# Optimization experiments

Measured on AMD Instinct MI355X. Metric: run time of the kernel, lower is better.

## Reference

```python
import jax, jax.numpy as jnp
import numpy as np

N, D, H = 50000, 256, 8
HD = D // H
E = 800000
NEG_SLOPE = 0.2


def setup_inputs() -> dict:
    key = jax.random.key(0)
    ks = jax.random.split(key, 12)
    s = 1.0 / np.sqrt(D)
    return {
        "x": jax.random.normal(ks[0], (N, D), jnp.float32),
        "edge_index": jax.random.randint(ks[1], (2, E), 0, N, jnp.int64),
        "edge_attr": jax.random.normal(ks[2], (E, 16), jnp.float32),
        # GATConv params: lin weight (no bias), attention vectors, output bias
        "W": jax.random.normal(ks[3], (D, D), jnp.float32) * s,
        "att_src": jax.random.normal(ks[4], (H, HD), jnp.float32) * s,
        "att_dst": jax.random.normal(ks[5], (H, HD), jnp.float32) * s,
        "bias": jnp.zeros((D,), jnp.float32),
        # LayerNorm
        "ln_g": jnp.ones((D,), jnp.float32),
        "ln_b": jnp.zeros((D,), jnp.float32),
        # FFN
        "W1": jax.random.normal(ks[6], (D, D), jnp.float32) * s,
        "b1": jnp.zeros((D,), jnp.float32),
        "W2": jax.random.normal(ks[7], (D, D), jnp.float32) * s,
        "b2": jnp.zeros((D,), jnp.float32),
    }


def _gat_layer(x, edge_index, W, att_src, att_dst, bias, ln_g, ln_b, W1, b1, W2, b2):
    n = x.shape[0]
    # GATConv default add_self_loops=True
    sl = jnp.arange(n, dtype=edge_index.dtype)
    src = jnp.concatenate([edge_index[0], sl])  # [E+N]
    dst = jnp.concatenate([edge_index[1], sl])  # [E+N]

    xp = (x @ W).reshape(n, H, HD)                      # [N,H,hd]
    a_src = jnp.einsum("nhd,hd->nh", xp, att_src)        # [N,H]
    a_dst = jnp.einsum("nhd,hd->nh", xp, att_dst)        # [N,H]

    e = a_src[src] + a_dst[dst]                          # [E+N,H]
    e = jax.nn.leaky_relu(e, NEG_SLOPE)
    # segment softmax over destination nodes (every node has a self loop)
    m = jax.ops.segment_max(e, dst, num_segments=n)      # [N,H]
    ex = jnp.exp(e - m[dst])
    denom = jax.ops.segment_sum(ex, dst, num_segments=n) # [N,H]
    alpha = ex / (denom[dst] + 1e-16)                    # [E+N,H]

    msg = alpha[:, :, None] * xp[src]                    # [E+N,H,hd]
    out = jax.ops.segment_sum(msg, dst, num_segments=n)  # [N,H,hd]
    h = out.reshape(n, D) + bias

    # residual + LayerNorm
    r = h + x
    mu = jnp.mean(r, axis=-1, keepdims=True)
    var = jnp.mean(jnp.square(r - mu), axis=-1, keepdims=True)
    hn = (r - mu) / jnp.sqrt(var + 1e-5) * ln_g + ln_b

    # FFN
    return jax.nn.relu(hn @ W1 + b1) @ W2 + b2


def reference(x, edge_index, edge_attr, W, att_src, att_dst, bias, ln_g, ln_b, W1, b1, W2, b2):
    # edge_attr is accepted but unused (GATConv built without edge_dim)
    return _gat_layer(x, edge_index, W, att_src, att_dst, bias, ln_g, ln_b, W1, b1, W2, b2)
```

## Files before the change

### kernel.cpp

```cpp
#include <hip/hip_runtime.h>
#include <hip/hip_bf16.h>

#define H 8
#define HD 32
#define DD 256
#define NEG_SLOPE 0.2f
#define SLOT 64

typedef short bf16x8 __attribute__((ext_vector_type(8)));
typedef float f32x4 __attribute__((ext_vector_type(4)));

__device__ __forceinline__ unsigned short f2bf(float f) {
    unsigned int u = __float_as_uint(f);
    unsigned int r = (u + 0x7fffu + ((u >> 16) & 1u)) >> 16;
    return (unsigned short)r;
}
__device__ __forceinline__ float bf2f(unsigned short b) {
    return __uint_as_float(((unsigned int)b) << 16);
}

#define GLOAD_LDS16(g, s)                                                        \
    __builtin_amdgcn_global_load_lds((const __attribute__((address_space(1))) void*)(g), \
                                     (__attribute__((address_space(3))) void*)(s), 16, 0, 0)

__global__ __launch_bounds__(256) void zero_cnt(int* __restrict__ cnt, int N) {
    int i = blockIdx.x * 256 + threadIdx.x;
    if (i < N) cnt[i] = 0;
}

__global__ __launch_bounds__(256) void prep(const float* __restrict__ x, unsigned short* __restrict__ xb,
                                            const float* __restrict__ W, unsigned short* __restrict__ Wt,
                                            const float* __restrict__ W1, unsigned short* __restrict__ W1t,
                                            const float* __restrict__ W2, unsigned short* __restrict__ W2t,
                                            const int* __restrict__ ei, int* __restrict__ src_sorted,
                                            int* __restrict__ cnt, int N, int n4, int E, int HB) {
    int b = blockIdx.x;
    int tid = threadIdx.x;
    if (b < HB) {
        int e = b * 256 + tid;
        if (e < E) {
            int s = ei[e];
            int d = ei[E + e];
            int r = atomicAdd(&cnt[d], 1);
            if (r < SLOT) src_sorted[(size_t)d * SLOT + r] = s;
        }
    } else if (b < HB + 768) {
        int wb = b - HB;
        const float* src = (wb < 256) ? W : (wb < 512) ? W1 : W2;
        unsigned short* dst = (wb < 256) ? Wt : (wb < 512) ? W1t : W2t;
        int i = (wb & 255) * 256 + tid;
        int n = i >> 8, k = i & 255;
        dst[i] = f2bf(src[k * 256 + n]);
    } else {
        int i = (b - HB - 768) * 256 + tid;
        if (i < n4) {
            float4 v = ((const float4*)x)[i];
            ushort4 o;
            o.x = f2bf(v.x); o.y = f2bf(v.y); o.z = f2bf(v.z); o.w = f2bf(v.w);
            ((ushort4*)xb)[i] = o;
        }
    }
}

template <bool ATTN, bool PHASE2>
__global__ __launch_bounds__(256) void gemm_fused(
    const unsigned short* __restrict__ A,
    const unsigned short* __restrict__ B1t, const float* __restrict__ b1,
    const unsigned short* __restrict__ B2t, const float* __restrict__ b2,
    void* __restrict__ Cout, int M,
    const float* __restrict__ att_s, const float* __restrict__ att_d,
    float* __restrict__ a_srcO, float* __restrict__ a_dstO) {
    __shared__ __align__(16) unsigned short Als[16384];
    __shared__ __align__(16) unsigned short t1ls[PHASE2 ? 64 * 280 : 8];

    const int tid = threadIdx.x;
    const int l = tid & 63;
    const int w = tid >> 6;
    const int r16 = l & 15, q0 = l >> 4;
    const int row0 = blockIdx.x * 64;

#pragma unroll
    for (int k = 0; k < 8; k++) {
        int c = k * 256 + tid;
        const unsigned short* g = A + (size_t)min(row0 + (c & 63), M - 1) * DD + (c >> 6) * 8;
        GLOAD_LDS16(g, &Als[c * 8]);
    }
    __syncthreads();

    f32x4 zero = {0.f, 0.f, 0.f, 0.f};
    f32x4 acc[4][4];
#pragma unroll
    for (int i = 0; i < 4; i++)
#pragma unroll
        for (int j = 0; j < 4; j++) acc[i][j] = zero;

#pragma unroll
    for (int kk = 0; kk < 4; kk++) {
#pragma unroll
        for (int t = 0; t < 2; t++) {
            const int qq = kk * 8 + t * 4 + q0;
            bf16x8 af[4], bf[4];
#pragma unroll
            for (int j = 0; j < 4; j++)
                bf[j] = *(const bf16x8*)&B1t[(size_t)(w * 64 + j * 16 + r16) * DD + qq * 8];
#pragma unroll
            for (int i = 0; i < 4; i++)
                af[i] = *(const bf16x8*)&Als[(qq * 64 + i * 16 + r16) * 8];
#pragma unroll
            for (int i = 0; i < 4; i++)
#pragma unroll
                for (int j = 0; j < 4; j++)
                    acc[i][j] = __builtin_amdgcn_mfma_f32_16x16x32_bf16(af[i], bf[j], acc[i][j], 0, 0, 0);
        }
    }

    if (!PHASE2) {
        float aws0, aws1, aws2, aws3, awd0, awd1, awd2, awd3;
        int hA = 0, hB = 0;
        if (ATTN) {
            hA = w * 2; hB = hA + 1;
            aws0 = att_s[hA * HD + r16];
            aws1 = att_s[hA * HD + 16 + r16];
            aws2 = att_s[hB * HD + r16];
            aws3 = att_s[hB * HD + 16 + r16];
            awd0 = att_d[hA * HD + r16];
            awd1 = att_d[hA * HD + 16 + r16];
            awd2 = att_d[hB * HD + r16];
            awd3 = att_d[hB * HD + 16 + r16];
        }
#pragma unroll
        for (int i = 0; i < 4; i++) {
#pragma unroll
            for (int r = 0; r < 4; r++) {
                int row = row0 + i * 16 + q0 * 4 + r;
                if (row < M) {
#pragma unroll
                    for (int j = 0; j < 4; j++) {
                        int col = w * 64 + j * 16 + r16;
                        ((unsigned short*)Cout)[(size_t)row * DD + col] = f2bf(acc[i][j][r]);
                    }
                }
                if (ATTN) {
                    float v0 = acc[i][0][r], v1 = acc[i][1][r];
                    float v2 = acc[i][2][r], v3 = acc[i][3][r];
                    float ps0 = v0 * aws0 + v1 * aws1;
                    float ps1 = v2 * aws2 + v3 * aws3;
                    float pd0 = v0 * awd0 + v1 * awd1;
                    float pd1 = v2 * awd2 + v3 * awd3;
#pragma unroll
                    for (int m = 1; m < 16; m <<= 1) {
                        ps0 += __shfl_xor(ps0, m, 64);
                        ps1 += __shfl_xor(ps1, m, 64);
                        pd0 += __shfl_xor(pd0, m, 64);
                        pd1 += __shfl_xor(pd1, m, 64);
                    }
                    if (r16 == 0 && row < M) {
                        a_srcO[row * H + hA] = ps0;
                        a_srcO[row * H + hB] = ps1;
                        a_dstO[row * H + hA] = pd0;
                        a_dstO[row * H + hB] = pd1;
                    }
                }
            }
        }
    } else {
        float bb1[4];
#pragma unroll
        for (int j = 0; j < 4; j++) bb1[j] = b1[w * 64 + j * 16 + r16];
#pragma unroll
        for (int i = 0; i < 4; i++)
#pragma unroll
            for (int r = 0; r < 4; r++) {
                int rl = i * 16 + q0 * 4 + r;
#pragma unroll
                for (int j = 0; j < 4; j++) {
                    float v = fmaxf(acc[i][j][r] + bb1[j], 0.f);
                    t1ls[rl * 280 + w * 64 + j * 16 + r16] = f2bf(v);
                }
            }
        __syncthreads();

#pragma unroll
        for (int i = 0; i < 4; i++)
#pragma unroll
            for (int j = 0; j < 4; j++) acc[i][j] = zero;

#pragma unroll
        for (int kk = 0; kk < 4; kk++) {
#pragma unroll
            for (int t = 0; t < 2; t++) {
                const int qq = kk * 8 + t * 4 + q0;
                bf16x8 af[4], bf[4];
#pragma unroll
                for (int j = 0; j < 4; j++)
                    bf[j] = *(const bf16x8*)&B2t[(size_t)(w * 64 + j * 16 + r16) * DD + qq * 8];
#pragma unroll
                for (int i = 0; i < 4; i++)
                    af[i] = *(const bf16x8*)&t1ls[(i * 16 + r16) * 280 + qq * 8];
#pragma unroll
                for (int i = 0; i < 4; i++)
#pragma unroll
                    for (int j = 0; j < 4; j++)
                        acc[i][j] = __builtin_amdgcn_mfma_f32_16x16x32_bf16(af[i], bf[j], acc[i][j], 0, 0, 0);
            }
        }

        float bb2[4];
#pragma unroll
        for (int j = 0; j < 4; j++) bb2[j] = b2[w * 64 + j * 16 + r16];
#pragma unroll
        for (int i = 0; i < 4; i++)
#pragma unroll
            for (int r = 0; r < 4; r++) {
                int row = row0 + i * 16 + q0 * 4 + r;
                if (row < M) {
#pragma unroll
                    for (int j = 0; j < 4; j++) {
                        int col = w * 64 + j * 16 + r16;
                        ((float*)Cout)[(size_t)row * DD + col] = acc[i][j][r] + bb2[j];
                    }
                }
            }
    }
}

__global__ __launch_bounds__(256) void aggregate_ln(
    const unsigned short* __restrict__ xp, const unsigned short* __restrict__ x_bf,
    const float* __restrict__ a_src, const float* __restrict__ a_dst,
    const int* __restrict__ cnt, const int* __restrict__ src_sorted,
    const float* __restrict__ bias, const float* __restrict__ ln_g,
    const float* __restrict__ ln_b, unsigned short* __restrict__ hn, int N) {
    int wave = threadIdx.x >> 6;
    int lane = threadIdx.x & 63;
    int n = blockIdx.x * 4 + wave;
    if (n >= N) return;
    int h = lane >> 3;

    float adst = a_dst[n * H + h];
    float e0 = a_src[n * H + h] + adst;
    e0 = (e0 > 0.f) ? e0 : NEG_SLOPE * e0;
    float ex = __expf(e0);
    ushort4 u = *(const ushort4*)(xp + (size_t)n * DD + lane * 4);
    float acc0 = ex * bf2f(u.x), acc1 = ex * bf2f(u.y);
    float acc2 = ex * bf2f(u.z), acc3 = ex * bf2f(u.w);
    float denom = ex;

    int beg = n * SLOT;
    int end = beg + cnt[n];
    int i = beg;
    for (; i + 7 < end; i += 8) {
        int s[8];
        float es[8];
        ushort4 uu[8];
#pragma unroll
        for (int k = 0; k < 8; k++) s[k] = src_sorted[i + k];
#pragma unroll
        for (int k = 0; k < 8; k++) es[k] = a_src[s[k] * H + h];
#pragma unroll
        for (int k = 0; k < 8; k++) uu[k] = *(const ushort4*)(xp + (size_t)s[k] * DD + lane * 4);
#pragma unroll
        for (int k = 0; k < 8; k++) {
            float e = es[k] + adst;
            e = (e > 0.f) ? e : NEG_SLOPE * e;
            float wk = __expf(e);
            acc0 += wk * bf2f(uu[k].x);
            acc1 += wk * bf2f(uu[k].y);
            acc2 += wk * bf2f(uu[k].z);
            acc3 += wk * bf2f(uu[k].w);
            denom += wk;
        }
    }
    for (; i < end; i++) {
        int s0 = src_sorted[i];
        float es0 = a_src[s0 * H + h];
        ushort4 u0 = *(const ushort4*)(xp + (size_t)s0 * DD + lane * 4);
        float e0a = es0 + adst;
        e0a = (e0a > 0.f) ? e0a : NEG_SLOPE * e0a;
        float w0 = __expf(e0a);
        acc0 += w0 * bf2f(u0.x);
        acc1 += w0 * bf2f(u0.y);
        acc2 += w0 * bf2f(u0.z);
        acc3 += w0 * bf2f(u0.w);
        denom += w0;
    }
    float inv = 1.f / (denom + 1e-16f);
    float4 bb = *(const float4*)(bias + lane * 4);
    ushort4 xr = *(const ushort4*)(x_bf + (size_t)n * DD + lane * 4);
    float r0 = acc0 * inv + bb.x + bf2f(xr.x);
    float r1 = acc1 * inv + bb.y + bf2f(xr.y);
    float r2 = acc2 * inv + bb.z + bf2f(xr.z);
    float r3 = acc3 * inv + bb.w + bf2f(xr.w);

    float s = r0 + r1 + r2 + r3;
#pragma unroll
    for (int m = 1; m < 64; m <<= 1) s += __shfl_xor(s, m, 64);
    float mu = s * (1.f / 256.f);
    float d0 = r0 - mu, d1 = r1 - mu, d2 = r2 - mu, d3 = r3 - mu;
    float qv = d0 * d0 + d1 * d1 + d2 * d2 + d3 * d3;
#pragma unroll
    for (int m = 1; m < 64; m <<= 1) qv += __shfl_xor(qv, m, 64);
    float rstd = rsqrtf(qv * (1.f / 256.f) + 1e-5f);
    float4 g = *(const float4*)(ln_g + lane * 4);
    float4 b = *(const float4*)(ln_b + lane * 4);
    ushort4 o;
    o.x = f2bf(d0 * rstd * g.x + b.x);
    o.y = f2bf(d1 * rstd * g.y + b.y);
    o.z = f2bf(d2 * rstd * g.z + b.z);
    o.w = f2bf(d3 * rstd * g.w + b.w);
    *(ushort4*)(hn + (size_t)n * DD + lane * 4) = o;
}

extern "C" void kernel_launch(void* const* d_in, const int* in_sizes, int n_in,
                              void* d_out, int out_size, void* d_ws, size_t ws_size,
                              hipStream_t stream) {
    const float* x = (const float*)d_in[0];
    const int* edge_index = (const int*)d_in[1];
    const float* W = (const float*)d_in[3];
    const float* att_src = (const float*)d_in[4];
    const float* att_dst = (const float*)d_in[5];
    const float* bias = (const float*)d_in[6];
    const float* ln_g = (const float*)d_in[7];
    const float* ln_b = (const float*)d_in[8];
    const float* W1 = (const float*)d_in[9];
    const float* b1 = (const float*)d_in[10];
    const float* W2 = (const float*)d_in[11];
    const float* b2 = (const float*)d_in[12];

    const int N = in_sizes[0] / DD;
    const int E = in_sizes[1] / 2;

    char* p = (char*)d_ws;
    auto carve = [&](size_t bytes) {
        char* r = p;
        p += (bytes + 255) & ~(size_t)255;
        return r;
    };
    unsigned short* x_bf = (unsigned short*)carve((size_t)N * DD * 2);
    unsigned short* xp_bf = (unsigned short*)carve((size_t)N * DD * 2);
    unsigned short* hn_bf = (unsigned short*)carve((size_t)N * DD * 2);
    float* a_src = (float*)carve((size_t)N * H * 4);
    float* a_dst = (float*)carve((size_t)N * H * 4);
    int* cnt = (int*)carve((size_t)N * 4);
    int* src_sorted = (int*)carve((size_t)N * SLOT * 4);
    unsigned short* Wt = (unsigned short*)carve(65536 * 2);
    unsigned short* W1t = (unsigned short*)carve(65536 * 2);
    unsigned short* W2t = (unsigned short*)carve(65536 * 2);

    const int n4 = N * DD / 4;
    const int HB = (E + 255) / 256;

    zero_cnt<<<(N + 255) / 256, 256, 0, stream>>>(cnt, N);

    int prep_blocks = HB + 768 + (n4 + 255) / 256;
    prep<<<prep_blocks, 256, 0, stream>>>(x, x_bf, W, Wt, W1, W1t, W2, W2t,
                                          edge_index, src_sorted, cnt, N, n4, E, HB);

    const int gblocks = (N + 63) / 64;

    gemm_fused<true, false><<<gblocks, 256, 0, stream>>>(
        x_bf, Wt, nullptr, nullptr, nullptr, xp_bf, N, att_src, att_dst, a_src, a_dst);

    aggregate_ln<<<(N + 3) / 4, 256, 0, stream>>>(xp_bf, x_bf, a_src, a_dst, cnt, src_sorted,
                                                  bias, ln_g, ln_b, hn_bf, N);

    gemm_fused<false, true><<<gblocks, 256, 0, stream>>>(
        hn_bf, W1t, b1, W2t, b2, d_out, N, nullptr, nullptr, nullptr, nullptr);
}
```

Measured before the change: 338.9 us.

## Replace fixed-slot atomic edge bucketing with two-level counting-sort CSR build

Replaces the per-destination fixed 64-slot adjacency, filled with global atomics per edge, with a two-pass bucketed counting sort: block-local histograms over 256-node buckets, a scan, a scatter into bucket order, then per-bucket local sorting into a compact CSR with rowPtr. This removes heavy global atomic contention and the sparse 64-slot layout, and it also removes the silent truncation for nodes with more than 64 in-edges. The cost is three extra kernel launches and an extra pass over the edges. Packing assumes source ids fit in 24 bits.

```diff
diff --git a/kernel.cpp b/kernel.cpp
--- a/kernel.cpp
+++ b/kernel.cpp
@@ -5,7 +5,8 @@
 #define HD 32
 #define DD 256
 #define NEG_SLOPE 0.2f
-#define SLOT 64
+#define EPB 4096
+#define NBMAX 256
 
 typedef short bf16x8 __attribute__((ext_vector_type(8)));
 typedef float f32x4 __attribute__((ext_vector_type(4)));
@@ -23,42 +24,124 @@
     __builtin_amdgcn_global_load_lds((const __attribute__((address_space(1))) void*)(g), \
                                      (__attribute__((address_space(3))) void*)(s), 16, 0, 0)
 
-__global__ __launch_bounds__(256) void zero_cnt(int* __restrict__ cnt, int N) {
-    int i = blockIdx.x * 256 + threadIdx.x;
-    if (i < N) cnt[i] = 0;
+__global__ __launch_bounds__(256) void zero_gc(int* __restrict__ gc) {
+    gc[threadIdx.x] = 0;
 }
 
 __global__ __launch_bounds__(256) void prep(const float* __restrict__ x, unsigned short* __restrict__ xb,
                                             const float* __restrict__ W, unsigned short* __restrict__ Wt,
                                             const float* __restrict__ W1, unsigned short* __restrict__ W1t,
                                             const float* __restrict__ W2, unsigned short* __restrict__ W2t,
-                                            const int* __restrict__ ei, int* __restrict__ src_sorted,
-                                            int* __restrict__ cnt, int N, int n4, int E, int HB) {
+                                            const int* __restrict__ ei, int* __restrict__ gc,
+                                            int* __restrict__ blockBase, int N, int n4, int E, int SB) {
+    __shared__ int lhist[NBMAX];
     int b = blockIdx.x;
     int tid = threadIdx.x;
-    if (b < HB) {
-        int e = b * 256 + tid;
-        if (e < E) {
-            int s = ei[e];
-            int d = ei[E + e];
-            int r = atomicAdd(&cnt[d], 1);
-            if (r < SLOT) src_sorted[(size_t)d * SLOT + r] = s;
-        }
-    } else if (b < HB + 768) {
-        int wb = b - HB;
+    if (b < SB) {
+        lhist[tid] = 0;
+        __syncthreads();
+        int e0 = b * EPB;
+#pragma unroll
+        for (int i = 0; i < 16; i++) {
+            int e = e0 + i * 256 + tid;
+            if (e < E) atomicAdd(&lhist[((unsigned)ei[E + e]) >> 8], 1);
+        }
+        __syncthreads();
+        int c = lhist[tid];
+        blockBase[b * NBMAX + tid] = c ? atomicAdd(&gc[tid], c) : 0;
+    } else if (b < SB + 768) {
+        int wb = b - SB;
         const float* src = (wb < 256) ? W : (wb < 512) ? W1 : W2;
         unsigned short* dst = (wb < 256) ? Wt : (wb < 512) ? W1t : W2t;
         int i = (wb & 255) * 256 + tid;
         int n = i >> 8, k = i & 255;
         dst[i] = f2bf(src[k * 256 + n]);
     } else {
-        int i = (b - HB - 768) * 256 + tid;
+        int i = (b - SB - 768) * 256 + tid;
         if (i < n4) {
             float4 v = ((const float4*)x)[i];
             ushort4 o;
             o.x = f2bf(v.x); o.y = f2bf(v.y); o.z = f2bf(v.z); o.w = f2bf(v.w);
             ((ushort4*)xb)[i] = o;
         }
+    }
+}
+
+__global__ __launch_bounds__(64) void scan_gc(const int* __restrict__ gc, int* __restrict__ bb) {
+    int lane = threadIdx.x;
+    int v[4], s = 0;
+#pragma unroll
+    for (int i = 0; i < 4; i++) { v[i] = gc[lane * 4 + i]; s += v[i]; }
+    int sc = s;
+#pragma unroll
+    for (int off = 1; off < 64; off <<= 1) {
+        int t = __shfl_up(sc, off, 64);
+        if (lane >= off) sc += t;
+    }
+    int run = sc - s;
+#pragma unroll
+    for (int i = 0; i < 4; i++) { bb[lane * 4 + i] = run; run += v[i]; }
+}
+
+__global__ __launch_bounds__(256) void bucket_scatter(const int* __restrict__ ei,
+                                                      const int* __restrict__ bb,
+                                                      const int* __restrict__ blockBase,
+                                                      unsigned int* __restrict__ tmp, int E) {
+    __shared__ int lrank[NBMAX];
+    int b = blockIdx.x;
+    int tid = threadIdx.x;
+    lrank[tid] = 0;
+    __syncthreads();
+    int e0 = b * EPB;
+#pragma unroll
+    for (int i = 0; i < 16; i++) {
+        int e = e0 + i * 256 + tid;
+        if (e < E) {
+            int s = ei[e];
+            unsigned d = (unsigned)ei[E + e];
+            int k = d >> 8;
+            int r = atomicAdd(&lrank[k], 1);
+            tmp[bb[k] + blockBase[b * NBMAX + k] + r] = ((d & 255u) << 24) | (unsigned)s;
+        }
+    }
+}
+
+__global__ __launch_bounds__(256) void bucket_csr(const unsigned int* __restrict__ tmp,
+                                                  const int* __restrict__ bb, const int* __restrict__ gc,
+                                                  int* __restrict__ src_sorted, int* __restrict__ rowPtr,
+                                                  int* __restrict__ cnt, int N) {
+    __shared__ int dh[NBMAX];
+    __shared__ int dbase[NBMAX];
+    __shared__ int dr[NBMAX];
+    int k = blockIdx.x;
+    int tid = threadIdx.x;
+    int base = bb[k];
+    int M = gc[k];
+    dh[tid] = 0;
+    dr[tid] = 0;
+    __syncthreads();
+    for (int i = tid; i < M; i += 256) atomicAdd(&dh[tmp[base + i] >> 24], 1);
+    __syncthreads();
+    int c = dh[tid];
+    dbase[tid] = c;
+    __syncthreads();
+    for (int off = 1; off < 256; off <<= 1) {
+        int add = (tid >= off) ? dbase[tid - off] : 0;
+        __syncthreads();
+        dbase[tid] += add;
+        __syncthreads();
+    }
+    int excl = dbase[tid] - c;
+    int d = (k << 8) + tid;
+    if (d < N) { cnt[d] = c; rowPtr[d] = base + excl; }
+    __syncthreads();
+    dbase[tid] = excl;
+    __syncthreads();
+    for (int i = tid; i < M; i += 256) {
+        unsigned p = tmp[base + i];
+        int dl = p >> 24;
+        int r = atomicAdd(&dr[dl], 1);
+        src_sorted[base + dbase[dl] + r] = (int)(p & 0xFFFFFFu);
     }
 }
 
@@ -227,7 +310,8 @@
 __global__ __launch_bounds__(256) void aggregate_ln(
     const unsigned short* __restrict__ xp, const unsigned short* __restrict__ x_bf,
     const float* __restrict__ a_src, const float* __restrict__ a_dst,
-    const int* __restrict__ cnt, const int* __restrict__ src_sorted,
+    const int* __restrict__ rowPtr, const int* __restrict__ cnt,
+    const int* __restrict__ src_sorted,
     const float* __restrict__ bias, const float* __restrict__ ln_g,
     const float* __restrict__ ln_b, unsigned short* __restrict__ hn, int N) {
     int wave = threadIdx.x >> 6;
@@ -245,7 +329,7 @@
     float acc2 = ex * bf2f(u.z), acc3 = ex * bf2f(u.w);
     float denom = ex;
 
-    int beg = n * SLOT;
+    int beg = rowPtr[n];
     int end = beg + cnt[n];
     int i = beg;
     for (; i + 7 < end; i += 8) {
@@ -340,28 +424,38 @@
     unsigned short* hn_bf = (unsigned short*)carve((size_t)N * DD * 2);
     float* a_src = (float*)carve((size_t)N * H * 4);
     float* a_dst = (float*)carve((size_t)N * H * 4);
+    int* gc = (int*)carve(NBMAX * 4);
+    int* bb = (int*)carve(NBMAX * 4);
+    int* rowPtr = (int*)carve((size_t)N * 4);
     int* cnt = (int*)carve((size_t)N * 4);
-    int* src_sorted = (int*)carve((size_t)N * SLOT * 4);
+    unsigned int* tmp = (unsigned int*)carve((size_t)E * 4);
+    int* src_sorted = (int*)carve((size_t)E * 4);
+    int* blockBase = (int*)carve((size_t)((E + EPB - 1) / EPB) * NBMAX * 4);
     unsigned short* Wt = (unsigned short*)carve(65536 * 2);
     unsigned short* W1t = (unsigned short*)carve(65536 * 2);
     unsigned short* W2t = (unsigned short*)carve(65536 * 2);
 
     const int n4 = N * DD / 4;
-    const int HB = (E + 255) / 256;
-
-    zero_cnt<<<(N + 255) / 256, 256, 0, stream>>>(cnt, N);
-
-    int prep_blocks = HB + 768 + (n4 + 255) / 256;
+    const int SB = (E + EPB - 1) / EPB;
+    const int NB = (N + 255) >> 8;
+
+    zero_gc<<<1, 256, 0, stream>>>(gc);
+
+    int prep_blocks = SB + 768 + (n4 + 255) / 256;
     prep<<<prep_blocks, 256, 0, stream>>>(x, x_bf, W, Wt, W1, W1t, W2, W2t,
-                                          edge_index, src_sorted, cnt, N, n4, E, HB);
+                                          edge_index, gc, blockBase, N, n4, E, SB);
+
+    scan_gc<<<1, 64, 0, stream>>>(gc, bb);
+    bucket_scatter<<<SB, 256, 0, stream>>>(edge_index, bb, blockBase, tmp, E);
+    bucket_csr<<<NB, 256, 0, stream>>>(tmp, bb, gc, src_sorted, rowPtr, cnt, N);
 
     const int gblocks = (N + 63) / 64;
 
     gemm_fused<true, false><<<gblocks, 256, 0, stream>>>(
         x_bf, Wt, nullptr, nullptr, nullptr, xp_bf, N, att_src, att_dst, a_src, a_dst);
 
-    aggregate_ln<<<(N + 3) / 4, 256, 0, stream>>>(xp_bf, x_bf, a_src, a_dst, cnt, src_sorted,
-                                                  bias, ln_g, ln_b, hn_bf, N);
+    aggregate_ln<<<(N + 3) / 4, 256, 0, stream>>>(xp_bf, x_bf, a_src, a_dst, rowPtr, cnt,
+                                                  src_sorted, bias, ln_g, ln_b, hn_bf, N);
 
     gemm_fused<false, true><<<gblocks, 256, 0, stream>>>(
         hn_bf, W1t, b1, W2t, b2, d_out, N, nullptr, nullptr, nullptr, nullptr);
```

Measured after the change: 331.1 us, median of 2. -2.3%, faster.
